# Kernel optimization log

Hardware: AMD Instinct MI355X
Metric: run time of the kernel (lower is better)

Reference implementation:

```python
import jax, jax.numpy as jnp
import numpy as np
import math

B, H, S, D = 8, 16, 1024, 64


def setup_inputs() -> dict:
    key = jax.random.key(0)
    kq, kk, kv, kl = jax.random.split(key, 4)
    queries = jax.random.normal(kq, (B * H, S, D), dtype=jnp.float32)
    keys = jax.random.normal(kk, (B * H, S, D), dtype=jnp.float32)
    values = jax.random.normal(kv, (B * H, S, D), dtype=jnp.float32)
    valid_lens = jax.random.randint(kl, (B,), 0, 1024, dtype=jnp.int64)
    return {"queries": queries, "keys": keys, "values": values, "valid_lens": valid_lens}


def reference(queries, keys, values, valid_lens):
    d = queries.shape[-1]
    seq_len = queries.shape[1]
    b = valid_lens.shape[0]
    h = queries.shape[0] // b
    scale = 1.0 / math.sqrt(d)
    # [BH, S, S] scores, faithful to bmm(q, k^T)/sqrt(d)
    scores = jnp.einsum("bqd,bkd->bqk", queries, keys) * scale
    # encode_mask: mask[b, q, k] = (k >= valid_lens[b]) for 1-D valid_lens
    key_mask = jnp.arange(seq_len) >= valid_lens[:, None]  # [B, S]
    scores = scores.reshape(b, h, seq_len, seq_len)
    # masked_fill with 1e-6 (NOT -inf), faithful to the original
    scores = jnp.where(key_mask[:, None, None, :], jnp.float32(1e-6), scores)
    attn = jax.nn.softmax(scores, axis=-1)
    out = jnp.einsum("bhqk,bhkd->bhqd", attn, values.reshape(b, h, seq_len, d))
    return out.reshape(b * h, seq_len, d)
```

## Files before the change

### kernel.cpp

```cpp
#include <hip/hip_runtime.h>
#include <hip/hip_bf16.h>

typedef short short4v __attribute__((ext_vector_type(4)));
typedef short short8v __attribute__((ext_vector_type(8)));
typedef float floatx4 __attribute__((ext_vector_type(4)));
typedef unsigned int uint2v __attribute__((ext_vector_type(2)));

#define SLEN 1024
#define DDIM 64
#define NBH  128

__device__ __forceinline__ unsigned short f2bf(float f) {
  union { float f; unsigned int u; } v; v.f = f;
  unsigned int u = v.u;
  u += 0x7fffu + ((u >> 16) & 1u);
  return (unsigned short)(u >> 16);
}

__device__ __forceinline__ unsigned int pkbf(float a, float b) {
  __hip_bfloat162 h = __float22bfloat162_rn(float2{a, b});
  union { __hip_bfloat162 h; unsigned int u; } c; c.h = h;
  return c.u;
}

__device__ __forceinline__ void pl32sw(unsigned int &a, unsigned int &b) {
#if __has_builtin(__builtin_amdgcn_permlane32_swap)
  uint2v r = __builtin_amdgcn_permlane32_swap(a, b, false, false);
  a = r[0]; b = r[1];
#else
  asm volatile("s_nop 1\n\tv_permlane32_swap_b32 %0, %1" : "+v"(a), "+v"(b));
#endif
}
__device__ __forceinline__ void pl16sw(unsigned int &a, unsigned int &b) {
#if __has_builtin(__builtin_amdgcn_permlane16_swap)
  uint2v r = __builtin_amdgcn_permlane16_swap(a, b, false, false);
  a = r[0]; b = r[1];
#else
  asm volatile("s_nop 1\n\tv_permlane16_swap_b32 %0, %1" : "+v"(a), "+v"(b));
#endif
}

__device__ __forceinline__ int decode_vl(const int* __restrict__ vraw, int bh) {
  const bool is64 = (vraw[1] == 0) && (vraw[3] == 0) && (vraw[5] == 0) && (vraw[7] == 0);
  const int b = bh >> 4;
  return is64 ? vraw[2 * b] : vraw[b];
}

__global__ __launch_bounds__(64)
void prep_cs(const float* __restrict__ Vg, float* __restrict__ CS,
             const int* __restrict__ vraw) {
  const int tile = blockIdx.x;
  const int bh = tile >> 4, ch = tile & 15;
  const int d = threadIdx.x;
  const int vl = decode_vl(vraw, bh);
  const int ts = (vl >> 6) + ((vl & 63) ? 1 : 0);
  float sum = 0.f;
  if (ch >= ts) {
    const float* src = Vg + (size_t)(bh * SLEN + ch * 64) * DDIM + d;
    float s0 = 0.f, s1 = 0.f, s2 = 0.f, s3 = 0.f;
    #pragma unroll
    for (int k = 0; k < 64; k += 4) {
      s0 += src[(size_t)(k + 0) * DDIM];
      s1 += src[(size_t)(k + 1) * DDIM];
      s2 += src[(size_t)(k + 2) * DDIM];
      s3 += src[(size_t)(k + 3) * DDIM];
    }
    sum = (s0 + s1) + (s2 + s3);
  }
  CS[(size_t)tile * 64 + d] = sum;
}

__global__ __launch_bounds__(64)
void prep_sv(float* __restrict__ CS, const int* __restrict__ vraw, int* __restrict__ SRT) {
  const int blk = blockIdx.x;
  if (blk < NBH) {
    const int d = threadIdx.x;
    float acc = 0.f;
    for (int ch = 15; ch >= 0; --ch) {
      const size_t idx = ((size_t)blk * 16 + ch) * 64 + d;
      acc += CS[idx];
      CS[idx] = acc;
    }
  } else {
    const int x = threadIdx.x;
    if (x < 8) {
      int key[16];
      #pragma unroll
      for (int k = 0; k < 16; ++k) {
        const int vv = decode_vl(vraw, x + 8 * k);
        key[k] = (vv >> 6) + ((vv & 63) ? 1 : 0);
      }
      #pragma unroll
      for (int i = 0; i < 16; ++i) {
        int rank = 0;
        #pragma unroll
        for (int k2 = 0; k2 < 16; ++k2)
          rank += (int)((key[k2] > key[i]) || (key[k2] == key[i] && k2 < i));
        SRT[x * 16 + rank] = x + 8 * i;
      }
    }
  }
}

__global__ __launch_bounds__(256)
void attn_main(const float* __restrict__ Qg, const float* __restrict__ Kg,
               const float* __restrict__ Vg, const float* __restrict__ SV,
               const int* __restrict__ SRT, const int* __restrict__ vraw,
               float* __restrict__ Og)
{
  __shared__ unsigned short K_lds[2][4096];
  __shared__ unsigned short VT_lds[2][4096];

  const int t  = threadIdx.x;
  const int ww = t >> 6;
  const int ln = t & 15;
  const int g  = (t >> 4) & 3;

  int bh, q0;
  if (SRT) {
    const int xcd  = blockIdx.x & 7;
    const int lidx = blockIdx.x >> 3;
    const int cu   = lidx & 31;
    const int j    = lidx >> 5;
    const int r    = j * 32 + ((j & 1) ? (31 - cu) : cu);
    bh = SRT[xcd * 16 + (r >> 3)];
    q0 = (r & 7) * 128;
  } else {
    bh = blockIdx.x & 127;
    q0 = (blockIdx.x >> 7) * 128;
  }

  const int vl          = decode_vl(vraw, bh);
  const int full_ch     = vl >> 6;
  const int has_partial = (vl & 63) ? 1 : 0;
  const int nch         = SV ? (full_ch + has_partial) : 16;
  const int tail_start  = full_ch + has_partial;

  const float qs = 0.125f * 1.44269504f;
  short8v bq[2][2];
  #pragma unroll
  for (int nt = 0; nt < 2; ++nt) {
    const float* qp = Qg + ((size_t)bh * SLEN + q0 + ww * 32 + nt * 16 + ln) * DDIM;
    #pragma unroll
    for (int st = 0; st < 2; ++st) {
      const float4 f0 = *(const float4*)(qp + st * 32 + g * 8);
      const float4 f1 = *(const float4*)(qp + st * 32 + g * 8 + 4);
      short8v a;
      a[0]=(short)f2bf(f0.x*qs); a[1]=(short)f2bf(f0.y*qs);
      a[2]=(short)f2bf(f0.z*qs); a[3]=(short)f2bf(f0.w*qs);
      a[4]=(short)f2bf(f1.x*qs); a[5]=(short)f2bf(f1.y*qs);
      a[6]=(short)f2bf(f1.z*qs); a[7]=(short)f2bf(f1.w*qs);
      bq[nt][st] = a;
    }
  }

  const int l7  = ln & 7;
  const int sw0 = ((g) ^ l7) * 8;
  const int sw1 = ((4 + g) ^ l7) * 8;

  short8v ones;
  #pragma unroll
  for (int j = 0; j < 8; ++j) ones[j] = (short)0x3F80;

  floatx4 ot[2][4], lacc[2];
  #pragma unroll
  for (int m = 0; m < 2; ++m) {
    lacc[m] = (floatx4){0.f, 0.f, 0.f, 0.f};
    #pragma unroll
    for (int f = 0; f < 4; ++f) ot[m][f] = (floatx4){0.f, 0.f, 0.f, 0.f};
  }

  float kr[2][8];
  float vlo[8], vhi[8];
  const int dv = t & 31;
  const int gv = t >> 5;

  const float* kbB = Kg + (size_t)bh * SLEN * DDIM;
  const float* vbB = Vg + (size_t)bh * SLEN * DDIM;

  auto stage_load = [&](int ch) {
    const float* kb_ = kbB + (size_t)ch * 64 * DDIM;
    const float* vb_ = vbB + (size_t)ch * 64 * DDIM;
    #pragma unroll
    for (int h = 0; h < 2; ++h) {
      const int q = t + h * 256;
      const int r = q >> 3, gr = q & 7;
      const float4 f0 = *(const float4*)(kb_ + r * DDIM + gr * 8);
      const float4 f1 = *(const float4*)(kb_ + r * DDIM + gr * 8 + 4);
      kr[h][0]=f0.x; kr[h][1]=f0.y; kr[h][2]=f0.z; kr[h][3]=f0.w;
      kr[h][4]=f1.x; kr[h][5]=f1.y; kr[h][6]=f1.z; kr[h][7]=f1.w;
    }
    #pragma unroll
    for (int j = 0; j < 8; ++j) {
      vlo[j] = vb_[(gv * 8 + j) * DDIM + dv];
      vhi[j] = vb_[(gv * 8 + j) * DDIM + dv + 32];
    }
  };
  auto stage_write = [&](int b) {
    #pragma unroll
    for (int h = 0; h < 2; ++h) {
      const int q = t + h * 256;
      const int r = q >> 3, gr = q & 7;
      union { short8v s; unsigned int u[4]; } ks;
      ks.u[0] = pkbf(kr[h][0], kr[h][1]);
      ks.u[1] = pkbf(kr[h][2], kr[h][3]);
      ks.u[2] = pkbf(kr[h][4], kr[h][5]);
      ks.u[3] = pkbf(kr[h][6], kr[h][7]);
      *(short8v*)&K_lds[b][r * 64 + ((gr ^ (r & 7)) * 8)] = ks.s;
    }
    union { short8v s; unsigned int u[4]; } va, vb2;
    va.u[0]  = pkbf(vlo[0], vlo[1]); va.u[1]  = pkbf(vlo[2], vlo[3]);
    va.u[2]  = pkbf(vlo[4], vlo[5]); va.u[3]  = pkbf(vlo[6], vlo[7]);
    vb2.u[0] = pkbf(vhi[0], vhi[1]); vb2.u[1] = pkbf(vhi[2], vhi[3]);
    vb2.u[2] = pkbf(vhi[4], vhi[5]); vb2.u[3] = pkbf(vhi[6], vhi[7]);
    const int swv = (gv ^ (dv & 7)) * 8;
    *(short8v*)&VT_lds[b][dv * 64 + swv] = va.s;
    *(short8v*)&VT_lds[b][(dv + 32) * 64 + swv] = vb2.s;
  };

  if (nch > 0) {
    stage_load(0);
    stage_write(0);
    if (nch > 1) stage_load(1);
    asm volatile("s_waitcnt lgkmcnt(0)" ::: "memory");
    __builtin_amdgcn_s_barrier();
    asm volatile("" ::: "memory");
  }

  for (int ch = 0; ch < nch; ++ch) {
    const int b = ch & 1;
    if (ch + 1 < nch) stage_write(b ^ 1);
    if (ch + 2 < nch) stage_load(ch + 2);

    floatx4 c[4][2];
    __builtin_amdgcn_s_setprio(1);
    #pragma unroll
    for (int mt = 0; mt < 4; ++mt) {
      const short8v a0 = *(const short8v*)&K_lds[b][(mt * 16 + ln) * 64 + sw0];
      const short8v a1 = *(const short8v*)&K_lds[b][(mt * 16 + ln) * 64 + sw1];
      #pragma unroll
      for (int nt = 0; nt < 2; ++nt) {
        floatx4 acc = (floatx4){0.f, 0.f, 0.f, 0.f};
        acc = __builtin_amdgcn_mfma_f32_16x16x32_bf16(a0, bq[nt][0], acc, 0, 0, 0);
        acc = __builtin_amdgcn_mfma_f32_16x16x32_bf16(a1, bq[nt][1], acc, 0, 0, 0);
        c[mt][nt] = acc;
      }
    }
    __builtin_amdgcn_s_setprio(0);

    unsigned int pk0[4][2], pk1[4][2];
    const bool fullv = (ch < full_ch);
    #pragma unroll
    for (int mt = 0; mt < 4; ++mt) {
      const int kg = ch * 64 + mt * 16 + g * 4;
      #pragma unroll
      for (int nt = 0; nt < 2; ++nt) {
        float p[4];
        if (fullv) {
          #pragma unroll
          for (int i = 0; i < 4; ++i) p[i] = __builtin_amdgcn_exp2f(c[mt][nt][i]);
        } else {
          #pragma unroll
          for (int i = 0; i < 4; ++i) {
            const float x = (kg + i < vl) ? c[mt][nt][i] : 0.0f;
            p[i] = __builtin_amdgcn_exp2f(x);
          }
        }
        pk0[mt][nt] = pkbf(p[0], p[1]);
        pk1[mt][nt] = pkbf(p[2], p[3]);
      }
    }

    short8v bp[2][2];
    #pragma unroll
    for (int st = 0; st < 2; ++st) {
      #pragma unroll
      for (int nt = 0; nt < 2; ++nt) {
        unsigned int a0 = pk0[2 * st][nt], b0 = pk0[2 * st + 1][nt];
        unsigned int a1 = pk1[2 * st][nt], b1 = pk1[2 * st + 1][nt];
        pl32sw(a0, b0); pl16sw(a0, b0);
        pl32sw(a1, b1); pl16sw(a1, b1);
        union { short8v s; unsigned int u[4]; } bb;
        bb.u[0] = a0; bb.u[1] = a1; bb.u[2] = b0; bb.u[3] = b1;
        bp[st][nt] = bb.s;
      }
    }

    __builtin_amdgcn_s_setprio(1);
    #pragma unroll
    for (int st = 0; st < 2; ++st) {
      lacc[0] = __builtin_amdgcn_mfma_f32_16x16x32_bf16(ones, bp[st][0], lacc[0], 0, 0, 0);
      lacc[1] = __builtin_amdgcn_mfma_f32_16x16x32_bf16(ones, bp[st][1], lacc[1], 0, 0, 0);
      const int sw = (st == 0) ? sw0 : sw1;
      #pragma unroll
      for (int f = 0; f < 4; ++f) {
        const short8v av = *(const short8v*)&VT_lds[b][(f * 16 + ln) * 64 + sw];
        ot[0][f] = __builtin_amdgcn_mfma_f32_16x16x32_bf16(av, bp[st][0], ot[0][f], 0, 0, 0);
        ot[1][f] = __builtin_amdgcn_mfma_f32_16x16x32_bf16(av, bp[st][1], ot[1][f], 0, 0, 0);
      }
    }
    __builtin_amdgcn_s_setprio(0);

    if (ch + 1 < nch) {
      asm volatile("s_waitcnt lgkmcnt(0)" ::: "memory");
      __builtin_amdgcn_s_barrier();
      asm volatile("" ::: "memory");
    }
  }

  if (SV != nullptr && tail_start < 16) {
    const float* sv = SV + ((size_t)bh * 16 + tail_start) * 64 + g * 4;
    float4 sv4[4];
    #pragma unroll
    for (int f = 0; f < 4; ++f) sv4[f] = *(const float4*)(sv + f * 16);
    const float ml = (float)(SLEN - tail_start * 64);
    #pragma unroll
    for (int nt = 0; nt < 2; ++nt) {
      #pragma unroll
      for (int i = 0; i < 4; ++i) lacc[nt][i] += ml;
      #pragma unroll
      for (int f = 0; f < 4; ++f) {
        ot[nt][f][0] += sv4[f].x; ot[nt][f][1] += sv4[f].y;
        ot[nt][f][2] += sv4[f].z; ot[nt][f][3] += sv4[f].w;
      }
    }
  }

  #pragma unroll
  for (int nt = 0; nt < 2; ++nt) {
    const float inv = 1.0f / lacc[nt][0];
    float* orow = Og + ((size_t)bh * SLEN + q0 + ww * 32 + nt * 16 + ln) * DDIM + g * 4;
    #pragma unroll
    for (int f = 0; f < 4; ++f) {
      float4 v4;
      v4.x = ot[nt][f][0] * inv; v4.y = ot[nt][f][1] * inv;
      v4.z = ot[nt][f][2] * inv; v4.w = ot[nt][f][3] * inv;
      *(float4*)(orow + f * 16) = v4;
    }
  }
}

extern "C" void kernel_launch(void* const* d_in, const int* in_sizes, int n_in,
                              void* d_out, int out_size, void* d_ws, size_t ws_size,
                              hipStream_t stream) {
  const float* Q = (const float*)d_in[0];
  const float* K = (const float*)d_in[1];
  const float* V = (const float*)d_in[2];
  const int*  vl = (const int*)d_in[3];
  float* out = (float*)d_out;

  const size_t ws_cs  = (size_t)NBH * 16 * 64 * 4;
  const size_t ws_all = ws_cs + 8 * 16 * 4;

  if (ws_size >= ws_all) {
    float* CS = (float*)d_ws;
    int*  SRT = (int*)((char*)d_ws + ws_cs);
    prep_cs<<<2048, 64, 0, stream>>>(V, CS, vl);
    prep_sv<<<NBH + 1, 64, 0, stream>>>(CS, vl, SRT);
    attn_main<<<dim3(1024), dim3(256), 0, stream>>>(Q, K, V, CS, SRT, vl, out);
  } else {
    attn_main<<<dim3(1024), dim3(256), 0, stream>>>(Q, K, V, nullptr, nullptr, vl, out);
  }
}
```

Measured before the change: 160.5 us.

## Replace static block-to-tile mapping with per-XCD atomic work queues and stealing

Blocks now pull tasks dynamically from per-XCD atomic counters, keyed by the hardware XCC_ID register, instead of using a fixed snake mapping from blockIdx. When a block's own XCD queue is empty it steals from the other XCDs. The aim is better load balance across tasks of very different lengths, since valid_lens vary. The cost is an atomic plus two __syncthreads per task, and correctness relies on XCC_ID matching the intended locality and on the grid covering every task.

Measured after the change: 251.7 us. +56.8%, slower.

```diff
diff --git a/kernel.cpp b/kernel.cpp
--- a/kernel.cpp
+++ b/kernel.cpp
@@ -38,6 +38,12 @@
 #else
   asm volatile("s_nop 1\n\tv_permlane16_swap_b32 %0, %1" : "+v"(a), "+v"(b));
 #endif
+}
+
+__device__ __forceinline__ int get_xcd() {
+  unsigned int x;
+  asm("s_getreg_b32 %0, hwreg(HW_REG_XCC_ID)" : "=s"(x));
+  return (int)(x & 7u);
 }
 
 __device__ __forceinline__ int decode_vl(const int* __restrict__ vraw, int bh) {
@@ -71,7 +77,8 @@
 }
 
 __global__ __launch_bounds__(64)
-void prep_sv(float* __restrict__ CS, const int* __restrict__ vraw, int* __restrict__ SRT) {
+void prep_sv(float* __restrict__ CS, const int* __restrict__ vraw,
+             int* __restrict__ SRT, int* __restrict__ QC) {
   const int blk = blockIdx.x;
   if (blk < NBH) {
     const int d = threadIdx.x;
@@ -84,6 +91,7 @@
   } else {
     const int x = threadIdx.x;
     if (x < 8) {
+      QC[x] = 0;
       int key[16];
       #pragma unroll
       for (int k = 0; k < 16; ++k) {
@@ -105,54 +113,19 @@
 __global__ __launch_bounds__(256)
 void attn_main(const float* __restrict__ Qg, const float* __restrict__ Kg,
                const float* __restrict__ Vg, const float* __restrict__ SV,
-               const int* __restrict__ SRT, const int* __restrict__ vraw,
-               float* __restrict__ Og)
+               const int* __restrict__ SRT, int* __restrict__ QC,
+               const int* __restrict__ vraw, float* __restrict__ Og)
 {
   __shared__ unsigned short K_lds[2][4096];
   __shared__ unsigned short VT_lds[2][4096];
+  __shared__ int task_s;
 
   const int t  = threadIdx.x;
   const int ww = t >> 6;
   const int ln = t & 15;
   const int g  = (t >> 4) & 3;
 
-  int bh, q0;
-  if (SRT) {
-    const int xcd  = blockIdx.x & 7;
-    const int lidx = blockIdx.x >> 3;
-    const int cu   = lidx & 31;
-    const int j    = lidx >> 5;
-    const int r    = j * 32 + ((j & 1) ? (31 - cu) : cu);
-    bh = SRT[xcd * 16 + (r >> 3)];
-    q0 = (r & 7) * 128;
-  } else {
-    bh = blockIdx.x & 127;
-    q0 = (blockIdx.x >> 7) * 128;
-  }
-
-  const int vl          = decode_vl(vraw, bh);
-  const int full_ch     = vl >> 6;
-  const int has_partial = (vl & 63) ? 1 : 0;
-  const int nch         = SV ? (full_ch + has_partial) : 16;
-  const int tail_start  = full_ch + has_partial;
-
-  const float qs = 0.125f * 1.44269504f;
-  short8v bq[2][2];
-  #pragma unroll
-  for (int nt = 0; nt < 2; ++nt) {
-    const float* qp = Qg + ((size_t)bh * SLEN + q0 + ww * 32 + nt * 16 + ln) * DDIM;
-    #pragma unroll
-    for (int st = 0; st < 2; ++st) {
-      const float4 f0 = *(const float4*)(qp + st * 32 + g * 8);
-      const float4 f1 = *(const float4*)(qp + st * 32 + g * 8 + 4);
-      short8v a;
-      a[0]=(short)f2bf(f0.x*qs); a[1]=(short)f2bf(f0.y*qs);
-      a[2]=(short)f2bf(f0.z*qs); a[3]=(short)f2bf(f0.w*qs);
-      a[4]=(short)f2bf(f1.x*qs); a[5]=(short)f2bf(f1.y*qs);
-      a[6]=(short)f2bf(f1.z*qs); a[7]=(short)f2bf(f1.w*qs);
-      bq[nt][st] = a;
-    }
-  }
+  const int xcd = SRT ? get_xcd() : 0;
 
   const int l7  = ln & 7;
   const int sw0 = ((g) ^ l7) * 8;
@@ -162,181 +135,233 @@
   #pragma unroll
   for (int j = 0; j < 8; ++j) ones[j] = (short)0x3F80;
 
-  floatx4 ot[2][4], lacc[2];
-  #pragma unroll
-  for (int m = 0; m < 2; ++m) {
-    lacc[m] = (floatx4){0.f, 0.f, 0.f, 0.f};
-    #pragma unroll
-    for (int f = 0; f < 4; ++f) ot[m][f] = (floatx4){0.f, 0.f, 0.f, 0.f};
-  }
-
-  float kr[2][8];
-  float vlo[8], vhi[8];
   const int dv = t & 31;
   const int gv = t >> 5;
 
-  const float* kbB = Kg + (size_t)bh * SLEN * DDIM;
-  const float* vbB = Vg + (size_t)bh * SLEN * DDIM;
-
-  auto stage_load = [&](int ch) {
-    const float* kb_ = kbB + (size_t)ch * 64 * DDIM;
-    const float* vb_ = vbB + (size_t)ch * 64 * DDIM;
+  for (;;) {
+    int bh, q0;
+    if (SRT) {
+      if (t == 0) {
+        int p = -1;
+        #pragma unroll 1
+        for (int i = 0; i < 8; ++i) {
+          const int qx = (xcd + i) & 7;
+          const int pos = atomicAdd(&QC[qx], 1);
+          if (pos < 128) { p = (qx << 7) | pos; break; }
+        }
+        task_s = p;
+      }
+      __syncthreads();
+      const int p = task_s;
+      __syncthreads();
+      if (p < 0) return;
+      const int qx = p >> 7, pos = p & 127;
+      bh = SRT[qx * 16 + (pos >> 3)];
+      q0 = (pos & 7) * 128;
+    } else {
+      bh = blockIdx.x & 127;
+      q0 = (blockIdx.x >> 7) * 128;
+    }
+
+    const int vl          = decode_vl(vraw, bh);
+    const int full_ch     = vl >> 6;
+    const int has_partial = (vl & 63) ? 1 : 0;
+    const int nch         = SV ? (full_ch + has_partial) : 16;
+    const int tail_start  = full_ch + has_partial;
+
+    const float qs = 0.125f * 1.44269504f;
+    short8v bq[2][2];
     #pragma unroll
-    for (int h = 0; h < 2; ++h) {
-      const int q = t + h * 256;
-      const int r = q >> 3, gr = q & 7;
-      const float4 f0 = *(const float4*)(kb_ + r * DDIM + gr * 8);
-      const float4 f1 = *(const float4*)(kb_ + r * DDIM + gr * 8 + 4);
-      kr[h][0]=f0.x; kr[h][1]=f0.y; kr[h][2]=f0.z; kr[h][3]=f0.w;
-      kr[h][4]=f1.x; kr[h][5]=f1.y; kr[h][6]=f1.z; kr[h][7]=f1.w;
-    }
+    for (int nt = 0; nt < 2; ++nt) {
+      const float* qp = Qg + ((size_t)bh * SLEN + q0 + ww * 32 + nt * 16 + ln) * DDIM;
+      #pragma unroll
+      for (int st = 0; st < 2; ++st) {
+        const float4 f0 = *(const float4*)(qp + st * 32 + g * 8);
+        const float4 f1 = *(const float4*)(qp + st * 32 + g * 8 + 4);
+        short8v a;
+        a[0]=(short)f2bf(f0.x*qs); a[1]=(short)f2bf(f0.y*qs);
+        a[2]=(short)f2bf(f0.z*qs); a[3]=(short)f2bf(f0.w*qs);
+        a[4]=(short)f2bf(f1.x*qs); a[5]=(short)f2bf(f1.y*qs);
+        a[6]=(short)f2bf(f1.z*qs); a[7]=(short)f2bf(f1.w*qs);
+        bq[nt][st] = a;
+      }
+    }
+
+    floatx4 ot[2][4], lacc[2];
     #pragma unroll
-    for (int j = 0; j < 8; ++j) {
-      vlo[j] = vb_[(gv * 8 + j) * DDIM + dv];
-      vhi[j] = vb_[(gv * 8 + j) * DDIM + dv + 32];
-    }
-  };
-  auto stage_write = [&](int b) {
-    #pragma unroll
-    for (int h = 0; h < 2; ++h) {
-      const int q = t + h * 256;
-      const int r = q >> 3, gr = q & 7;
-      union { short8v s; unsigned int u[4]; } ks;
-      ks.u[0] = pkbf(kr[h][0], kr[h][1]);
-      ks.u[1] = pkbf(kr[h][2], kr[h][3]);
-      ks.u[2] = pkbf(kr[h][4], kr[h][5]);
-      ks.u[3] = pkbf(kr[h][6], kr[h][7]);
-      *(short8v*)&K_lds[b][r * 64 + ((gr ^ (r & 7)) * 8)] = ks.s;
-    }
-    union { short8v s; unsigned int u[4]; } va, vb2;
-    va.u[0]  = pkbf(vlo[0], vlo[1]); va.u[1]  = pkbf(vlo[2], vlo[3]);
-    va.u[2]  = pkbf(vlo[4], vlo[5]); va.u[3]  = pkbf(vlo[6], vlo[7]);
-    vb2.u[0] = pkbf(vhi[0], vhi[1]); vb2.u[1] = pkbf(vhi[2], vhi[3]);
-    vb2.u[2] = pkbf(vhi[4], vhi[5]); vb2.u[3] = pkbf(vhi[6], vhi[7]);
-    const int swv = (gv ^ (dv & 7)) * 8;
-    *(short8v*)&VT_lds[b][dv * 64 + swv] = va.s;
-    *(short8v*)&VT_lds[b][(dv + 32) * 64 + swv] = vb2.s;
-  };
-
-  if (nch > 0) {
-    stage_load(0);
-    stage_write(0);
-    if (nch > 1) stage_load(1);
-    asm volatile("s_waitcnt lgkmcnt(0)" ::: "memory");
-    __builtin_amdgcn_s_barrier();
-    asm volatile("" ::: "memory");
-  }
-
-  for (int ch = 0; ch < nch; ++ch) {
-    const int b = ch & 1;
-    if (ch + 1 < nch) stage_write(b ^ 1);
-    if (ch + 2 < nch) stage_load(ch + 2);
-
-    floatx4 c[4][2];
-    __builtin_amdgcn_s_setprio(1);
-    #pragma unroll
-    for (int mt = 0; mt < 4; ++mt) {
-      const short8v a0 = *(const short8v*)&K_lds[b][(mt * 16 + ln) * 64 + sw0];
-      const short8v a1 = *(const short8v*)&K_lds[b][(mt * 16 + ln) * 64 + sw1];
-      #pragma unroll
-      for (int nt = 0; nt < 2; ++nt) {
-        floatx4 acc = (floatx4){0.f, 0.f, 0.f, 0.f};
-        acc = __builtin_amdgcn_mfma_f32_16x16x32_bf16(a0, bq[nt][0], acc, 0, 0, 0);
-        acc = __builtin_amdgcn_mfma_f32_16x16x32_bf16(a1, bq[nt][1], acc, 0, 0, 0);
-        c[mt][nt] = acc;
-      }
-    }
-    __builtin_amdgcn_s_setprio(0);
-
-    unsigned int pk0[4][2], pk1[4][2];
-    const bool fullv = (ch < full_ch);
-    #pragma unroll
-    for (int mt = 0; mt < 4; ++mt) {
-      const int kg = ch * 64 + mt * 16 + g * 4;
-      #pragma unroll
-      for (int nt = 0; nt < 2; ++nt) {
-        float p[4];
-        if (fullv) {
-          #pragma unroll
-          for (int i = 0; i < 4; ++i) p[i] = __builtin_amdgcn_exp2f(c[mt][nt][i]);
-        } else {
-          #pragma unroll
-          for (int i = 0; i < 4; ++i) {
-            const float x = (kg + i < vl) ? c[mt][nt][i] : 0.0f;
-            p[i] = __builtin_amdgcn_exp2f(x);
-          }
-        }
-        pk0[mt][nt] = pkbf(p[0], p[1]);
-        pk1[mt][nt] = pkbf(p[2], p[3]);
-      }
-    }
-
-    short8v bp[2][2];
-    #pragma unroll
-    for (int st = 0; st < 2; ++st) {
-      #pragma unroll
-      for (int nt = 0; nt < 2; ++nt) {
-        unsigned int a0 = pk0[2 * st][nt], b0 = pk0[2 * st + 1][nt];
-        unsigned int a1 = pk1[2 * st][nt], b1 = pk1[2 * st + 1][nt];
-        pl32sw(a0, b0); pl16sw(a0, b0);
-        pl32sw(a1, b1); pl16sw(a1, b1);
-        union { short8v s; unsigned int u[4]; } bb;
-        bb.u[0] = a0; bb.u[1] = a1; bb.u[2] = b0; bb.u[3] = b1;
-        bp[st][nt] = bb.s;
-      }
-    }
-
-    __builtin_amdgcn_s_setprio(1);
-    #pragma unroll
-    for (int st = 0; st < 2; ++st) {
-      lacc[0] = __builtin_amdgcn_mfma_f32_16x16x32_bf16(ones, bp[st][0], lacc[0], 0, 0, 0);
-      lacc[1] = __builtin_amdgcn_mfma_f32_16x16x32_bf16(ones, bp[st][1], lacc[1], 0, 0, 0);
-      const int sw = (st == 0) ? sw0 : sw1;
-      #pragma unroll
-      for (int f = 0; f < 4; ++f) {
-        const short8v av = *(const short8v*)&VT_lds[b][(f * 16 + ln) * 64 + sw];
-        ot[0][f] = __builtin_amdgcn_mfma_f32_16x16x32_bf16(av, bp[st][0], ot[0][f], 0, 0, 0);
-        ot[1][f] = __builtin_amdgcn_mfma_f32_16x16x32_bf16(av, bp[st][1], ot[1][f], 0, 0, 0);
-      }
-    }
-    __builtin_amdgcn_s_setprio(0);
-
-    if (ch + 1 < nch) {
+    for (int m = 0; m < 2; ++m) {
+      lacc[m] = (floatx4){0.f, 0.f, 0.f, 0.f};
+      #pragma unroll
+      for (int f = 0; f < 4; ++f) ot[m][f] = (floatx4){0.f, 0.f, 0.f, 0.f};
+    }
+
+    float kr[2][8];
+    float vlo[8], vhi[8];
+    const float* kbB = Kg + (size_t)bh * SLEN * DDIM;
+    const float* vbB = Vg + (size_t)bh * SLEN * DDIM;
+
+    auto stage_load = [&](int ch) {
+      const float* kb_ = kbB + (size_t)ch * 64 * DDIM;
+      const float* vb_ = vbB + (size_t)ch * 64 * DDIM;
+      #pragma unroll
+      for (int h = 0; h < 2; ++h) {
+        const int q = t + h * 256;
+        const int r = q >> 3, gr = q & 7;
+        const float4 f0 = *(const float4*)(kb_ + r * DDIM + gr * 8);
+        const float4 f1 = *(const float4*)(kb_ + r * DDIM + gr * 8 + 4);
+        kr[h][0]=f0.x; kr[h][1]=f0.y; kr[h][2]=f0.z; kr[h][3]=f0.w;
+        kr[h][4]=f1.x; kr[h][5]=f1.y; kr[h][6]=f1.z; kr[h][7]=f1.w;
+      }
+      #pragma unroll
+      for (int j = 0; j < 8; ++j) {
+        vlo[j] = vb_[(gv * 8 + j) * DDIM + dv];
+        vhi[j] = vb_[(gv * 8 + j) * DDIM + dv + 32];
+      }
+    };
+    auto stage_write = [&](int b) {
+      #pragma unroll
+      for (int h = 0; h < 2; ++h) {
+        const int q = t + h * 256;
+        const int r = q >> 3, gr = q & 7;
+        union { short8v s; unsigned int u[4]; } ks;
+        ks.u[0] = pkbf(kr[h][0], kr[h][1]);
+        ks.u[1] = pkbf(kr[h][2], kr[h][3]);
+        ks.u[2] = pkbf(kr[h][4], kr[h][5]);
+        ks.u[3] = pkbf(kr[h][6], kr[h][7]);
+        *(short8v*)&K_lds[b][r * 64 + ((gr ^ (r & 7)) * 8)] = ks.s;
+      }
+      union { short8v s; unsigned int u[4]; } va, vb2;
+      va.u[0]  = pkbf(vlo[0], vlo[1]); va.u[1]  = pkbf(vlo[2], vlo[3]);
+      va.u[2]  = pkbf(vlo[4], vlo[5]); va.u[3]  = pkbf(vlo[6], vlo[7]);
+      vb2.u[0] = pkbf(vhi[0], vhi[1]); vb2.u[1] = pkbf(vhi[2], vhi[3]);
+      vb2.u[2] = pkbf(vhi[4], vhi[5]); vb2.u[3] = pkbf(vhi[6], vhi[7]);
+      const int swv = (gv ^ (dv & 7)) * 8;
+      *(short8v*)&VT_lds[b][dv * 64 + swv] = va.s;
+      *(short8v*)&VT_lds[b][(dv + 32) * 64 + swv] = vb2.s;
+    };
+
+    if (nch > 0) {
+      stage_load(0);
+      stage_write(0);
+      if (nch > 1) stage_load(1);
       asm volatile("s_waitcnt lgkmcnt(0)" ::: "memory");
       __builtin_amdgcn_s_barrier();
       asm volatile("" ::: "memory");
     }
-  }
-
-  if (SV != nullptr && tail_start < 16) {
-    const float* sv = SV + ((size_t)bh * 16 + tail_start) * 64 + g * 4;
-    float4 sv4[4];
-    #pragma unroll
-    for (int f = 0; f < 4; ++f) sv4[f] = *(const float4*)(sv + f * 16);
-    const float ml = (float)(SLEN - tail_start * 64);
+
+    for (int ch = 0; ch < nch; ++ch) {
+      const int b = ch & 1;
+      if (ch + 1 < nch) stage_write(b ^ 1);
+      if (ch + 2 < nch) stage_load(ch + 2);
+
+      floatx4 c[4][2];
+      __builtin_amdgcn_s_setprio(1);
+      #pragma unroll
+      for (int mt = 0; mt < 4; ++mt) {
+        const short8v a0 = *(const short8v*)&K_lds[b][(mt * 16 + ln) * 64 + sw0];
+        const short8v a1 = *(const short8v*)&K_lds[b][(mt * 16 + ln) * 64 + sw1];
+        #pragma unroll
+        for (int nt = 0; nt < 2; ++nt) {
+          floatx4 acc = (floatx4){0.f, 0.f, 0.f, 0.f};
+          acc = __builtin_amdgcn_mfma_f32_16x16x32_bf16(a0, bq[nt][0], acc, 0, 0, 0);
+          acc = __builtin_amdgcn_mfma_f32_16x16x32_bf16(a1, bq[nt][1], acc, 0, 0, 0);
+          c[mt][nt] = acc;
+        }
+      }
+      __builtin_amdgcn_s_setprio(0);
+
+      unsigned int pk0[4][2], pk1[4][2];
+      const bool fullv = (ch < full_ch);
+      #pragma unroll
+      for (int mt = 0; mt < 4; ++mt) {
+        const int kg = ch * 64 + mt * 16 + g * 4;
+        #pragma unroll
+        for (int nt = 0; nt < 2; ++nt) {
+          float p[4];
+          if (fullv) {
+            #pragma unroll
+            for (int i = 0; i < 4; ++i) p[i] = __builtin_amdgcn_exp2f(c[mt][nt][i]);
+          } else {
+            #pragma unroll
+            for (int i = 0; i < 4; ++i) {
+              const float x = (kg + i < vl) ? c[mt][nt][i] : 0.0f;
+              p[i] = __builtin_amdgcn_exp2f(x);
+            }
+          }
+          pk0[mt][nt] = pkbf(p[0], p[1]);
+          pk1[mt][nt] = pkbf(p[2], p[3]);
+        }
+      }
+
+      short8v bp[2][2];
+      #pragma unroll
+      for (int st = 0; st < 2; ++st) {
+        #pragma unroll
+        for (int nt = 0; nt < 2; ++nt) {
+          unsigned int a0 = pk0[2 * st][nt], b0 = pk0[2 * st + 1][nt];
+          unsigned int a1 = pk1[2 * st][nt], b1 = pk1[2 * st + 1][nt];
+          pl32sw(a0, b0); pl16sw(a0, b0);
+          pl32sw(a1, b1); pl16sw(a1, b1);
+          union { short8v s; unsigned int u[4]; } bb;
+          bb.u[0] = a0; bb.u[1] = a1; bb.u[2] = b0; bb.u[3] = b1;
+          bp[st][nt] = bb.s;
+        }
+      }
+
+      __builtin_amdgcn_s_setprio(1);
+      #pragma unroll
+      for (int st = 0; st < 2; ++st) {
+        lacc[0] = __builtin_amdgcn_mfma_f32_16x16x32_bf16(ones, bp[st][0], lacc[0], 0, 0, 0);
+        lacc[1] = __builtin_amdgcn_mfma_f32_16x16x32_bf16(ones, bp[st][1], lacc[1], 0, 0, 0);
+        const int sw = (st == 0) ? sw0 : sw1;
+        #pragma unroll
+        for (int f = 0; f < 4; ++f) {
+          const short8v av = *(const short8v*)&VT_lds[b][(f * 16 + ln) * 64 + sw];
+          ot[0][f] = __builtin_amdgcn_mfma_f32_16x16x32_bf16(av, bp[st][0], ot[0][f], 0, 0, 0);
+          ot[1][f] = __builtin_amdgcn_mfma_f32_16x16x32_bf16(av, bp[st][1], ot[1][f], 0, 0, 0);
+        }
+      }
+      __builtin_amdgcn_s_setprio(0);
+
+      if (ch + 1 < nch) {
+        asm volatile("s_waitcnt lgkmcnt(0)" ::: "memory");
+        __builtin_amdgcn_s_barrier();
+        asm volatile("" ::: "memory");
+      }
+    }
+
+    if (SV != nullptr && tail_start < 16) {
+      const float* sv = SV + ((size_t)bh * 16 + tail_start) * 64 + g * 4;
+      float4 sv4[4];
+      #pragma unroll
+      for (int f = 0; f < 4; ++f) sv4[f] = *(const float4*)(sv + f * 16);
+      const float ml = (float)(SLEN - tail_start * 64);
+      #pragma unroll
+      for (int nt = 0; nt < 2; ++nt) {
+        #pragma unroll
+        for (int i = 0; i < 4; ++i) lacc[nt][i] += ml;
+        #pragma unroll
+        for (int f = 0; f < 4; ++f) {
+          ot[nt][f][0] += sv4[f].x; ot[nt][f][1] += sv4[f].y;
+          ot[nt][f][2] += sv4[f].z; ot[nt][f][3] += sv4[f].w;
+        }
+      }
+    }
+
     #pragma unroll
     for (int nt = 0; nt < 2; ++nt) {
-      #pragma unroll
-      for (int i = 0; i < 4; ++i) lacc[nt][i] += ml;
+      const float inv = 1.0f / lacc[nt][0];
+      float* orow = Og + ((size_t)bh * SLEN + q0 + ww * 32 + nt * 16 + ln) * DDIM + g * 4;
       #pragma unroll
       for (int f = 0; f < 4; ++f) {
-        ot[nt][f][0] += sv4[f].x; ot[nt][f][1] += sv4[f].y;
-        ot[nt][f][2] += sv4[f].z; ot[nt][f][3] += sv4[f].w;
-      }
-    }
-  }
-
-  #pragma unroll
-  for (int nt = 0; nt < 2; ++nt) {
-    const float inv = 1.0f / lacc[nt][0];
-    float* orow = Og + ((size_t)bh * SLEN + q0 + ww * 32 + nt * 16 + ln) * DDIM + g * 4;
-    #pragma unroll
-    for (int f = 0; f < 4; ++f) {
-      float4 v4;
-      v4.x = ot[nt][f][0] * inv; v4.y = ot[nt][f][1] * inv;
-      v4.z = ot[nt][f][2] * inv; v4.w = ot[nt][f][3] * inv;
-      *(float4*)(orow + f * 16) = v4;
-    }
+        float4 v4;
+        v4.x = ot[nt][f][0] * inv; v4.y = ot[nt][f][1] * inv;
+        v4.z = ot[nt][f][2] * inv; v4.w = ot[nt][f][3] * inv;
+        *(float4*)(orow + f * 16) = v4;
+      }
+    }
+
+    if (!SRT) return;
   }
 }
 
@@ -350,15 +375,17 @@
   float* out = (float*)d_out;
 
   const size_t ws_cs  = (size_t)NBH * 16 * 64 * 4;
-  const size_t ws_all = ws_cs + 8 * 16 * 4;
+  const size_t ws_srt = ws_cs + 8 * 16 * 4;
+  const size_t ws_all = ws_srt + 8 * 4;
 
   if (ws_size >= ws_all) {
-    float* CS = (float*)d_ws;
-    int*  SRT = (int*)((char*)d_ws + ws_cs);
+    float* CS  = (float*)d_ws;
+    int*  SRT  = (int*)((char*)d_ws + ws_cs);
+    int*  QC   = (int*)((char*)d_ws + ws_srt);
     prep_cs<<<2048, 64, 0, stream>>>(V, CS, vl);
-    prep_sv<<<NBH + 1, 64, 0, stream>>>(CS, vl, SRT);
-    attn_main<<<dim3(1024), dim3(256), 0, stream>>>(Q, K, V, CS, SRT, vl, out);
+    prep_sv<<<NBH + 1, 64, 0, stream>>>(CS, vl, SRT, QC);
+    attn_main<<<dim3(1024), dim3(256), 0, stream>>>(Q, K, V, CS, SRT, QC, vl, out);
   } else {
-    attn_main<<<dim3(1024), dim3(256), 0, stream>>>(Q, K, V, nullptr, nullptr, vl, out);
+    attn_main<<<dim3(1024), dim3(256), 0, stream>>>(Q, K, V, nullptr, nullptr, nullptr, vl, out);
   }
 }
```

## Split KV range of longest heads across two blocks and combine partials

Applied to the files above, without the earlier changes.

Sorts all 128 heads globally by valid chunk count and, for the 48 heaviest, splits each 128-query tile's key range into two halves handled by separate blocks, which write unnormalized partial outputs and row sums to workspace. A new combine kernel sums the two partials and normalizes. This is meant to fix load imbalance, where blocks for long-sequence heads dominate the tail of the grid. In exchange it adds an extra kernel launch, partial-output traffic through global memory, and drops the XCD-aware block-to-CU mapping used before.

Result: slower. 193.6 us (+20.6%).

```diff
diff --git a/kernel.cpp b/kernel.cpp
--- a/kernel.cpp
+++ b/kernel.cpp
@@ -9,6 +9,8 @@
 #define SLEN 1024
 #define DDIM 64
 #define NBH  128
+#define NSPLIT 48
+#define NTASK  (NSPLIT * 16 + (NBH - NSPLIT) * 8)
 
 __device__ __forceinline__ unsigned short f2bf(float f) {
   union { float f; unsigned int u; } v; v.f = f;
@@ -45,6 +47,10 @@
   const int b = bh >> 4;
   return is64 ? vraw[2 * b] : vraw[b];
 }
+__device__ __forceinline__ int nch_of(const int* __restrict__ vraw, int bh) {
+  const int v = decode_vl(vraw, bh);
+  return (v >> 6) + ((v & 63) ? 1 : 0);
+}
 
 __global__ __launch_bounds__(64)
 void prep_cs(const float* __restrict__ Vg, float* __restrict__ CS,
@@ -52,8 +58,7 @@
   const int tile = blockIdx.x;
   const int bh = tile >> 4, ch = tile & 15;
   const int d = threadIdx.x;
-  const int vl = decode_vl(vraw, bh);
-  const int ts = (vl >> 6) + ((vl & 63) ? 1 : 0);
+  const int ts = nch_of(vraw, bh);
   float sum = 0.f;
   if (ch >= ts) {
     const float* src = Vg + (size_t)(bh * SLEN + ch * 64) * DDIM + d;
@@ -71,7 +76,8 @@
 }
 
 __global__ __launch_bounds__(64)
-void prep_sv(float* __restrict__ CS, const int* __restrict__ vraw, int* __restrict__ SRT) {
+void prep_sv(float* __restrict__ CS, const int* __restrict__ vraw,
+             int* __restrict__ GSRT, int4* __restrict__ TL) {
   const int blk = blockIdx.x;
   if (blk < NBH) {
     const int d = threadIdx.x;
@@ -82,21 +88,33 @@
       CS[idx] = acc;
     }
   } else {
+    __shared__ int gs[NBH];
     const int x = threadIdx.x;
-    if (x < 8) {
-      int key[16];
-      #pragma unroll
-      for (int k = 0; k < 16; ++k) {
-        const int vv = decode_vl(vraw, x + 8 * k);
-        key[k] = (vv >> 6) + ((vv & 63) ? 1 : 0);
-      }
-      #pragma unroll
-      for (int i = 0; i < 16; ++i) {
-        int rank = 0;
-        #pragma unroll
-        for (int k2 = 0; k2 < 16; ++k2)
-          rank += (int)((key[k2] > key[i]) || (key[k2] == key[i] && k2 < i));
-        SRT[x * 16 + rank] = x + 8 * i;
+    for (int i = x; i < NBH; i += 64) {
+      const int ni = nch_of(vraw, i);
+      int rank = 0;
+      for (int j = 0; j < NBH; ++j) {
+        const int nj = nch_of(vraw, j);
+        rank += (int)((nj > ni) || (nj == ni && j < i));
+      }
+      gs[rank] = i;
+    }
+    __syncthreads();
+    for (int r = x; r < NBH; r += 64) {
+      const int bh = gs[r];
+      GSRT[r] = bh;
+      const int nn = nch_of(vraw, bh);
+      if (r < NSPLIT) {
+        const int h = (nn + 1) >> 1;
+        for (int qb = 0; qb < 8; ++qb) {
+          const int sl = (r * 8 + qb) * 2;
+          TL[r * 16 + qb * 2]     = make_int4(bh | (qb << 8),             0, h,  sl);
+          TL[r * 16 + qb * 2 + 1] = make_int4(bh | (qb << 8) | (1 << 13), h, nn, sl + 1);
+        }
+      } else {
+        for (int qb = 0; qb < 8; ++qb)
+          TL[NSPLIT * 16 + (r - NSPLIT) * 8 + qb] =
+              make_int4(bh | (qb << 8) | (1 << 12) | (1 << 13), 0, nn, 0);
       }
     }
   }
@@ -105,8 +123,8 @@
 __global__ __launch_bounds__(256)
 void attn_main(const float* __restrict__ Qg, const float* __restrict__ Kg,
                const float* __restrict__ Vg, const float* __restrict__ SV,
-               const int* __restrict__ SRT, const int* __restrict__ vraw,
-               float* __restrict__ Og)
+               const int4* __restrict__ TL, const int* __restrict__ vraw,
+               float* __restrict__ Og, float* __restrict__ PO, float* __restrict__ PL)
 {
   __shared__ unsigned short K_lds[2][4096];
   __shared__ unsigned short VT_lds[2][4096];
@@ -116,24 +134,25 @@
   const int ln = t & 15;
   const int g  = (t >> 4) & 3;
 
-  int bh, q0;
-  if (SRT) {
-    const int xcd  = blockIdx.x & 7;
-    const int lidx = blockIdx.x >> 3;
-    const int cu   = lidx & 31;
-    const int j    = lidx >> 5;
-    const int r    = j * 32 + ((j & 1) ? (31 - cu) : cu);
-    bh = SRT[xcd * 16 + (r >> 3)];
-    q0 = (r & 7) * 128;
+  int bh, q0, ch0, ch1, slot;
+  bool direct, tailf;
+  if (TL) {
+    const int4 te = TL[blockIdx.x];
+    bh = te.x & 127;
+    q0 = ((te.x >> 8) & 7) * 128;
+    direct = ((te.x >> 12) & 1) != 0;
+    tailf  = ((te.x >> 13) & 1) != 0;
+    ch0 = te.y; ch1 = te.z; slot = te.w;
   } else {
+    if (blockIdx.x >= 1024) return;
     bh = blockIdx.x & 127;
     q0 = (blockIdx.x >> 7) * 128;
+    ch0 = 0; ch1 = 16; slot = 0; direct = true; tailf = false;
   }
 
   const int vl          = decode_vl(vraw, bh);
   const int full_ch     = vl >> 6;
   const int has_partial = (vl & 63) ? 1 : 0;
-  const int nch         = SV ? (full_ch + has_partial) : 16;
   const int tail_start  = full_ch + has_partial;
 
   const float qs = 0.125f * 1.44269504f;
@@ -174,7 +193,6 @@
   float vlo[8], vhi[8];
   const int dv = t & 31;
   const int gv = t >> 5;
-
   const float* kbB = Kg + (size_t)bh * SLEN * DDIM;
   const float* vbB = Vg + (size_t)bh * SLEN * DDIM;
 
@@ -218,19 +236,21 @@
     *(short8v*)&VT_lds[b][(dv + 32) * 64 + swv] = vb2.s;
   };
 
-  if (nch > 0) {
-    stage_load(0);
+  const int cnt = ch1 - ch0;
+  if (cnt > 0) {
+    stage_load(ch0);
     stage_write(0);
-    if (nch > 1) stage_load(1);
+    if (cnt > 1) stage_load(ch0 + 1);
     asm volatile("s_waitcnt lgkmcnt(0)" ::: "memory");
     __builtin_amdgcn_s_barrier();
     asm volatile("" ::: "memory");
   }
 
-  for (int ch = 0; ch < nch; ++ch) {
-    const int b = ch & 1;
-    if (ch + 1 < nch) stage_write(b ^ 1);
-    if (ch + 2 < nch) stage_load(ch + 2);
+  for (int k = 0; k < cnt; ++k) {
+    const int ch = ch0 + k;
+    const int b = k & 1;
+    if (k + 1 < cnt) stage_write(b ^ 1);
+    if (k + 2 < cnt) stage_load(ch0 + k + 2);
 
     floatx4 c[4][2];
     __builtin_amdgcn_s_setprio(1);
@@ -301,14 +321,14 @@
     }
     __builtin_amdgcn_s_setprio(0);
 
-    if (ch + 1 < nch) {
+    if (k + 1 < cnt) {
       asm volatile("s_waitcnt lgkmcnt(0)" ::: "memory");
       __builtin_amdgcn_s_barrier();
       asm volatile("" ::: "memory");
     }
   }
 
-  if (SV != nullptr && tail_start < 16) {
+  if (tailf && SV != nullptr && tail_start < 16) {
     const float* sv = SV + ((size_t)bh * 16 + tail_start) * 64 + g * 4;
     float4 sv4[4];
     #pragma unroll
@@ -326,17 +346,62 @@
     }
   }
 
+  if (direct) {
+    #pragma unroll
+    for (int nt = 0; nt < 2; ++nt) {
+      const float inv = 1.0f / lacc[nt][0];
+      float* orow = Og + ((size_t)bh * SLEN + q0 + ww * 32 + nt * 16 + ln) * DDIM + g * 4;
+      #pragma unroll
+      for (int f = 0; f < 4; ++f) {
+        float4 v4;
+        v4.x = ot[nt][f][0] * inv; v4.y = ot[nt][f][1] * inv;
+        v4.z = ot[nt][f][2] * inv; v4.w = ot[nt][f][3] * inv;
+        *(float4*)(orow + f * 16) = v4;
+      }
+    }
+  } else {
+    float* po = PO + (size_t)slot * (128 * 64);
+    float* pl = PL + (size_t)slot * 128;
+    #pragma unroll
+    for (int nt = 0; nt < 2; ++nt) {
+      const int row = ww * 32 + nt * 16 + ln;
+      float* prow = po + row * 64 + g * 4;
+      #pragma unroll
+      for (int f = 0; f < 4; ++f) {
+        float4 v4;
+        v4.x = ot[nt][f][0]; v4.y = ot[nt][f][1];
+        v4.z = ot[nt][f][2]; v4.w = ot[nt][f][3];
+        *(float4*)(prow + f * 16) = v4;
+      }
+      if (g == 0) pl[row] = lacc[nt][0];
+    }
+  }
+}
+
+__global__ __launch_bounds__(256)
+void combine_po(const int* __restrict__ GSRT, const float* __restrict__ PO,
+                const float* __restrict__ PL, float* __restrict__ Og) {
+  const int r   = blockIdx.x >> 3;
+  const int q0b = blockIdx.x & 7;
+  const int bh  = GSRT[r];
+  const int t   = threadIdx.x;
+  const int row = t >> 1;
+  const int seg = t & 1;
+  const int s0  = blockIdx.x * 2, s1 = s0 + 1;
+  const float la = PL[(size_t)s0 * 128 + row];
+  const float lb = PL[(size_t)s1 * 128 + row];
+  const float inv = 1.0f / (la + lb);
+  const float* pa = PO + (size_t)s0 * (128 * 64) + row * 64 + seg * 32;
+  const float* pb = PO + (size_t)s1 * (128 * 64) + row * 64 + seg * 32;
+  float* og = Og + ((size_t)bh * SLEN + q0b * 128 + row) * DDIM + seg * 32;
   #pragma unroll
-  for (int nt = 0; nt < 2; ++nt) {
-    const float inv = 1.0f / lacc[nt][0];
-    float* orow = Og + ((size_t)bh * SLEN + q0 + ww * 32 + nt * 16 + ln) * DDIM + g * 4;
-    #pragma unroll
-    for (int f = 0; f < 4; ++f) {
-      float4 v4;
-      v4.x = ot[nt][f][0] * inv; v4.y = ot[nt][f][1] * inv;
-      v4.z = ot[nt][f][2] * inv; v4.w = ot[nt][f][3] * inv;
-      *(float4*)(orow + f * 16) = v4;
-    }
+  for (int j = 0; j < 8; ++j) {
+    const float4 a4 = *(const float4*)(pa + j * 4);
+    const float4 b4 = *(const float4*)(pb + j * 4);
+    float4 o4;
+    o4.x = (a4.x + b4.x) * inv; o4.y = (a4.y + b4.y) * inv;
+    o4.z = (a4.z + b4.z) * inv; o4.w = (a4.w + b4.w) * inv;
+    *(float4*)(og + j * 4) = o4;
   }
 }
 
@@ -349,16 +414,24 @@
   const int*  vl = (const int*)d_in[3];
   float* out = (float*)d_out;
 
-  const size_t ws_cs  = (size_t)NBH * 16 * 64 * 4;
-  const size_t ws_all = ws_cs + 8 * 16 * 4;
+  const size_t off_gsrt = (size_t)NBH * 16 * 64 * 4;
+  const size_t off_tl   = off_gsrt + NBH * 4;
+  const size_t off_pl   = off_tl + (size_t)NTASK * 16;
+  const size_t off_po   = off_pl + (size_t)NSPLIT * 8 * 2 * 128 * 4;
+  const size_t ws_all   = off_po + (size_t)NSPLIT * 8 * 2 * 128 * 64 * 4;
 
   if (ws_size >= ws_all) {
-    float* CS = (float*)d_ws;
-    int*  SRT = (int*)((char*)d_ws + ws_cs);
+    float* CS   = (float*)d_ws;
+    int*   GSRT = (int*)((char*)d_ws + off_gsrt);
+    int4*  TL   = (int4*)((char*)d_ws + off_tl);
+    float* PL   = (float*)((char*)d_ws + off_pl);
+    float* PO   = (float*)((char*)d_ws + off_po);
     prep_cs<<<2048, 64, 0, stream>>>(V, CS, vl);
-    prep_sv<<<NBH + 1, 64, 0, stream>>>(CS, vl, SRT);
-    attn_main<<<dim3(1024), dim3(256), 0, stream>>>(Q, K, V, CS, SRT, vl, out);
+    prep_sv<<<NBH + 1, 64, 0, stream>>>(CS, vl, GSRT, TL);
+    attn_main<<<dim3(NTASK), dim3(256), 0, stream>>>(Q, K, V, CS, TL, vl, out, PO, PL);
+    combine_po<<<dim3(NSPLIT * 8), dim3(256), 0, stream>>>(GSRT, PO, PL, out);
   } else {
-    attn_main<<<dim3(1024), dim3(256), 0, stream>>>(Q, K, V, nullptr, nullptr, vl, out);
-  }
-}
+    attn_main<<<dim3(1024), dim3(256), 0, stream>>>(Q, K, V, nullptr, nullptr, vl, out,
+                                                    nullptr, nullptr);
+  }
+}
```

## Merge prep kernels and replace XCD-aware schedule with global sorted tile list

Applied to the files above, without the earlier changes.

Two preprocessing kernels (per-chunk V column sums plus a suffix scan, and a per-XCD sort) become one kernel. It computes only the masked-tail V sum per head and a global descending-work ordering of all 128 heads, written out as a tile list. Dropping one launch and the intermediate per-chunk buffer cuts prep overhead. The main kernel now reads its (head, query-block) from the list in block-ID order instead of the XCD/CU-aware serpentine mapping, which changes load balancing and L2 locality across XCDs.

Result: slower. 165.3 us (+3.0%).

```diff
diff --git a/kernel.cpp b/kernel.cpp
--- a/kernel.cpp
+++ b/kernel.cpp
@@ -45,59 +45,47 @@
   const int b = bh >> 4;
   return is64 ? vraw[2 * b] : vraw[b];
 }
-
-__global__ __launch_bounds__(64)
-void prep_cs(const float* __restrict__ Vg, float* __restrict__ CS,
-             const int* __restrict__ vraw) {
-  const int tile = blockIdx.x;
-  const int bh = tile >> 4, ch = tile & 15;
-  const int d = threadIdx.x;
-  const int vl = decode_vl(vraw, bh);
-  const int ts = (vl >> 6) + ((vl & 63) ? 1 : 0);
-  float sum = 0.f;
-  if (ch >= ts) {
-    const float* src = Vg + (size_t)(bh * SLEN + ch * 64) * DDIM + d;
-    float s0 = 0.f, s1 = 0.f, s2 = 0.f, s3 = 0.f;
-    #pragma unroll
-    for (int k = 0; k < 64; k += 4) {
-      s0 += src[(size_t)(k + 0) * DDIM];
-      s1 += src[(size_t)(k + 1) * DDIM];
-      s2 += src[(size_t)(k + 2) * DDIM];
-      s3 += src[(size_t)(k + 3) * DDIM];
-    }
-    sum = (s0 + s1) + (s2 + s3);
-  }
-  CS[(size_t)tile * 64 + d] = sum;
-}
-
-__global__ __launch_bounds__(64)
-void prep_sv(float* __restrict__ CS, const int* __restrict__ vraw, int* __restrict__ SRT) {
-  const int blk = blockIdx.x;
-  if (blk < NBH) {
-    const int d = threadIdx.x;
-    float acc = 0.f;
-    for (int ch = 15; ch >= 0; --ch) {
-      const size_t idx = ((size_t)blk * 16 + ch) * 64 + d;
-      acc += CS[idx];
-      CS[idx] = acc;
-    }
+__device__ __forceinline__ int nch_of(const int* __restrict__ vraw, int bh) {
+  const int v = decode_vl(vraw, bh);
+  return (v >> 6) + ((v & 63) ? 1 : 0);
+}
+
+__global__ __launch_bounds__(256)
+void prep(const float* __restrict__ Vg, const int* __restrict__ vraw,
+          float* __restrict__ SV2, int* __restrict__ TL) {
+  if (blockIdx.x < NBH) {
+    const int bh = blockIdx.x;
+    const int d  = threadIdx.x & 63;
+    const int cg = threadIdx.x >> 6;
+    const int ts = nch_of(vraw, bh);
+    float sum = 0.f;
+    for (int ch = ts + cg; ch < 16; ch += 4) {
+      const float* src = Vg + (size_t)(bh * SLEN + ch * 64) * DDIM + d;
+      #pragma unroll
+      for (int k = 0; k < 64; ++k) sum += src[(size_t)k * DDIM];
+    }
+    __shared__ float red[4][64];
+    red[cg][d] = sum;
+    __syncthreads();
+    if (cg == 0)
+      SV2[(size_t)bh * 64 + d] = (red[0][d] + red[1][d]) + (red[2][d] + red[3][d]);
   } else {
+    __shared__ int gs[NBH];
     const int x = threadIdx.x;
-    if (x < 8) {
-      int key[16];
-      #pragma unroll
-      for (int k = 0; k < 16; ++k) {
-        const int vv = decode_vl(vraw, x + 8 * k);
-        key[k] = (vv >> 6) + ((vv & 63) ? 1 : 0);
-      }
-      #pragma unroll
-      for (int i = 0; i < 16; ++i) {
-        int rank = 0;
-        #pragma unroll
-        for (int k2 = 0; k2 < 16; ++k2)
-          rank += (int)((key[k2] > key[i]) || (key[k2] == key[i] && k2 < i));
-        SRT[x * 16 + rank] = x + 8 * i;
-      }
+    if (x < NBH) {
+      const int ni = nch_of(vraw, x);
+      int rank = 0;
+      for (int j = 0; j < NBH; ++j) {
+        const int nj = nch_of(vraw, j);
+        rank += (int)((nj > ni) || (nj == ni && j < x));
+      }
+      gs[rank] = x;
+    }
+    __syncthreads();
+    if (x < NBH) {
+      const int bh = gs[x];
+      #pragma unroll
+      for (int qb = 0; qb < 8; ++qb) TL[x * 8 + qb] = bh | (qb << 8);
     }
   }
 }
@@ -105,7 +93,7 @@
 __global__ __launch_bounds__(256)
 void attn_main(const float* __restrict__ Qg, const float* __restrict__ Kg,
                const float* __restrict__ Vg, const float* __restrict__ SV,
-               const int* __restrict__ SRT, const int* __restrict__ vraw,
+               const int* __restrict__ TL, const int* __restrict__ vraw,
                float* __restrict__ Og)
 {
   __shared__ unsigned short K_lds[2][4096];
@@ -117,14 +105,10 @@
   const int g  = (t >> 4) & 3;
 
   int bh, q0;
-  if (SRT) {
-    const int xcd  = blockIdx.x & 7;
-    const int lidx = blockIdx.x >> 3;
-    const int cu   = lidx & 31;
-    const int j    = lidx >> 5;
-    const int r    = j * 32 + ((j & 1) ? (31 - cu) : cu);
-    bh = SRT[xcd * 16 + (r >> 3)];
-    q0 = (r & 7) * 128;
+  if (TL) {
+    const int te = TL[blockIdx.x];
+    bh = te & 127;
+    q0 = ((te >> 8) & 7) * 128;
   } else {
     bh = blockIdx.x & 127;
     q0 = (blockIdx.x >> 7) * 128;
@@ -174,7 +158,6 @@
   float vlo[8], vhi[8];
   const int dv = t & 31;
   const int gv = t >> 5;
-
   const float* kbB = Kg + (size_t)bh * SLEN * DDIM;
   const float* vbB = Vg + (size_t)bh * SLEN * DDIM;
 
@@ -309,7 +292,7 @@
   }
 
   if (SV != nullptr && tail_start < 16) {
-    const float* sv = SV + ((size_t)bh * 16 + tail_start) * 64 + g * 4;
+    const float* sv = SV + (size_t)bh * 64 + g * 4;
     float4 sv4[4];
     #pragma unroll
     for (int f = 0; f < 4; ++f) sv4[f] = *(const float4*)(sv + f * 16);
@@ -349,15 +332,14 @@
   const int*  vl = (const int*)d_in[3];
   float* out = (float*)d_out;
 
-  const size_t ws_cs  = (size_t)NBH * 16 * 64 * 4;
-  const size_t ws_all = ws_cs + 8 * 16 * 4;
+  const size_t off_tl = (size_t)NBH * 64 * 4;
+  const size_t ws_all = off_tl + 1024 * 4;
 
   if (ws_size >= ws_all) {
-    float* CS = (float*)d_ws;
-    int*  SRT = (int*)((char*)d_ws + ws_cs);
-    prep_cs<<<2048, 64, 0, stream>>>(V, CS, vl);
-    prep_sv<<<NBH + 1, 64, 0, stream>>>(CS, vl, SRT);
-    attn_main<<<dim3(1024), dim3(256), 0, stream>>>(Q, K, V, CS, SRT, vl, out);
+    float* SV2 = (float*)d_ws;
+    int*   TL  = (int*)((char*)d_ws + off_tl);
+    prep<<<NBH + 1, 256, 0, stream>>>(V, vl, SV2, TL);
+    attn_main<<<dim3(1024), dim3(256), 0, stream>>>(Q, K, V, SV2, TL, vl, out);
   } else {
     attn_main<<<dim3(1024), dim3(256), 0, stream>>>(Q, K, V, nullptr, nullptr, vl, out);
   }
```
